# Kernel tuning notes

Hardware: AMD Instinct MI355X
Metric: run time of the kernel (lower is better)

Reference implementation:

```python
import jax, jax.numpy as jnp
from jax import lax
import numpy as np

PARAM_NAMES = ['S1_max','S2_max','f_tens','f_rchr','f_base','r1','ku','c','alpha','psi','kappa','ki','ks','n','v','v_A','v_B','Ac_max','b','lambda','chi','mu_t','T_rain','T_melt','melt_rate','lapse_rate','opg','MFMAX','MFMIN']
PARAM_BOUNDS = {'S1_max':(50.,5000.),'S2_max':(100.,10000.),'f_tens':(.05,.95),'f_rchr':(.05,.95),'f_base':(.05,.95),'r1':(.05,.95),'ku':(.01,1000.),'c':(1.,20.),'alpha':(1.,250.),'psi':(1.,5.),'kappa':(.05,.95),'ki':(.01,1000.),'ks':(.001,10000.),'n':(1.,10.),'v':(.001,.25),'v_A':(.001,.25),'v_B':(.001,.25),'Ac_max':(.05,.95),'b':(.001,3.),'lambda':(5.,10.),'chi':(2.,5.),'mu_t':(.01,5.),'T_rain':(-2.,4.),'T_melt':(-2.,4.),'melt_rate':(1.,10.),'lapse_rate':(-9.8,0.),'opg':(0.,1.),'MFMAX':(1.,10.),'MFMIN':(0.,10.)}
_LOW = jnp.asarray(np.array([PARAM_BOUNDS[n][0] for n in PARAM_NAMES], np.float32))
_HIGH = jnp.asarray(np.array([PARAM_BOUNDS[n][1] for n in PARAM_NAMES], np.float32))
_IDX = {n: i for i, n in enumerate(PARAM_NAMES)}
REF_ELEV = 1500.0      # reference gauge elevation [m]
ROUTE_SHAPE = 2.5      # gamma unit-hydrograph shape
UH_LEN = 30            # routing kernel length [days]


def setup_inputs() -> dict:
    key = jax.random.key(0)
    k1, k2, k3 = jax.random.split(key, 3)
    E, T, NB = 64, 8192, 16
    raw_params = 0.5 * jax.random.normal(k1, (E, 29), jnp.float32)
    u = jax.random.uniform(k2, (T, 3), jnp.float32)
    precip = jnp.where(u[:, 0] > 0.6, (u[:, 0] - 0.6) * 50.0, 0.0)  # mm/day
    pet = u[:, 1] * 5.0                                             # mm/day
    temp = (u[:, 2] - 0.4) * 25.0                                   # deg C
    forcing = jnp.stack([precip, pet, temp], axis=1)
    state_init = jnp.array([50.0, 250.0], jnp.float32)
    af = jax.random.uniform(k3, (NB,), jnp.float32) + 0.1
    area_frac = af / af.sum()
    mean_elev = 800.0 + 150.0 * jnp.arange(NB, dtype=jnp.float32)
    return dict(raw_params=raw_params, forcing=forcing, state_init=state_init,
                area_frac=area_frac, mean_elev=mean_elev)


def _simulate(raw_params, forcing, state_init, area_frac, mean_elev):
    phys = _LOW + (_HIGH - _LOW) * jax.nn.sigmoid(raw_params)  # [E,29] sigmoid-bounded params
    g = lambda n: phys[:, _IDX[n]][:, None]                    # [E,1]
    s1max, s2max = g('S1_max'), g('S2_max')
    ku, c_exp, ki = g('ku'), g('c'), g('ki')
    ks, n_exp = g('ks')[:, 0], g('n')[:, 0]
    ac_max, b_exp = g('Ac_max'), g('b')
    t_rain, t_melt, melt_rate = g('T_rain'), g('T_melt'), g('melt_rate')
    delev = (mean_elev - REF_ELEV) / 1000.0                    # [nb] km
    tshift = g('lapse_rate') * delev                           # [E,nb]
    pmult = jnp.maximum(1.0 + g('opg') * delev, 0.0)           # [E,nb]
    s2max1 = g('S2_max')[:, 0]
    E, NB = raw_params.shape[0], mean_elev.shape[0]

    swe0 = jnp.zeros((E, NB), phys.dtype)
    s1_0 = jnp.broadcast_to(state_init[0], (E, NB))
    s2_0 = jnp.broadcast_to(state_init[1], (E,))

    def step(carry, x):
        swe, s1, s2 = carry
        p, pet, tair = x[0], x[1], x[2]
        tb = tair + tshift                                     # band temperature [E,nb]
        pb = p * pmult                                         # band precip
        rain = jnp.where(tb > t_rain, pb, 0.0)
        snow = pb - rain
        melt = jnp.minimum(melt_rate * jnp.maximum(tb - t_melt, 0.0), swe + snow)
        swe = swe + snow - melt
        infl = rain + melt
        w1 = jnp.clip(s1 / s1max, 0.0, 1.0)
        evap = pet * w1
        qsx = ac_max * w1 ** b_exp * infl                      # saturated-area runoff
        perc = ku * w1 ** c_exp                                # percolation to lower zone
        qif = ki * w1                                          # interflow
        s1n = s1 + infl - qsx - evap - perc - qif
        over1 = jnp.maximum(s1n - s1max, 0.0)
        s1 = jnp.clip(s1n, 0.0, s1max)
        qsurf = qsx + over1
        rech = jnp.sum(area_frac * perc, axis=-1)              # [E]
        w2 = jnp.clip(s2 / s2max1, 0.0, 1.0)
        qb = ks * w2 ** n_exp                                  # baseflow
        s2n = s2 + rech - qb
        over2 = jnp.maximum(s2n - s2max1, 0.0)
        s2 = jnp.clip(s2n, 0.0, s2max1)
        q = jnp.sum(area_frac * (qsurf + qif), axis=-1) + qb + over2
        return (swe, s1, s2), q

    _, runoff = lax.scan(step, (swe0, s1_0, s2_0), forcing)   # [T,E]
    runoff = runoff.T                                          # [E,T]

    # gamma unit-hydrograph routing: shape=ROUTE_SHAPE, scale=mu_t
    delay = phys[:, _IDX['mu_t']]                              # [E]
    tmid = jnp.arange(UH_LEN, dtype=runoff.dtype) + 0.5        # bin midpoints [days]
    k = jnp.asarray(ROUTE_SHAPE, runoff.dtype)
    logpdf = ((k - 1.0) * jnp.log(tmid)[None, :]
              - tmid[None, :] / delay[:, None]
              - lax.lgamma(k) - k * jnp.log(delay)[:, None])
    w = jnp.exp(logpdf)
    w = w / w.sum(axis=1, keepdims=True)                       # [E,UH_LEN]
    T = runoff.shape[1]
    padded = jnp.pad(runoff, ((0, 0), (UH_LEN - 1, 0)))
    routed = jnp.zeros_like(runoff)
    for l in range(UH_LEN):  # small fixed kernel loop (not a data-dim loop)
        routed = routed + w[:, l:l + 1] * lax.dynamic_slice_in_dim(padded, UH_LEN - 1 - l, T, axis=1)
    return routed


def reference(raw_params, forcing, state_init, area_frac, mean_elev):
    return _simulate(raw_params, forcing, state_init, area_frac, mean_elev)
```

## Files before the change

kernel.cpp:

```cpp
#include <hip/hip_runtime.h>
#include <math.h>

#define T_STEPS 8192
#define GROUP   64
#define NQ      (GROUP / 4)
#define NG      (T_STEPS / GROUP)

__device__ __forceinline__ float hw_exp2(float x) { return __builtin_amdgcn_exp2f(x); }
__device__ __forceinline__ float hw_log2(float x) { return __builtin_amdgcn_logf(x); }

#if __has_builtin(__builtin_amdgcn_fmed3f)
__device__ __forceinline__ float clamp01(float x) { return __builtin_amdgcn_fmed3f(x, 0.0f, 1.0f); }
#else
__device__ __forceinline__ float clamp01(float x) { return fminf(fmaxf(x, 0.0f), 1.0f); }
#endif

__global__ __launch_bounds__(256, 1) void fuse_pipe_kernel(
    const float* __restrict__ raw,
    const float* __restrict__ forcing,
    const float* __restrict__ state_init,
    const float* __restrict__ area_frac,
    const float* __restrict__ mean_elev,
    float* __restrict__ qout)
{
    const int tid  = threadIdx.x;
    const int wid  = tid >> 6;
    const int lane = tid & 63;
    const int grp  = lane >> 4;
    const int nb   = lane & 15;
    const int e    = blockIdx.x * 4 + grp;

    __shared__ float4 bufI4[2][NQ][64];
    __shared__ float4 bufC4[2][NQ][64];
    __shared__ float4 bufP4[2][NQ][67];
    __shared__ float4 bufQ4[2][NQ][67];
    __shared__ float4 bufR4[2][4][NQ + 1];
    __shared__ float4 bufS4[2][4][NQ + 1];

    const float* rp = raw + e * 29;
    auto phys = [&](int idx, float lo, float hi) {
        float x = rp[idx];
        float s = 1.0f / (1.0f + expf(-x));
        return lo + (hi - lo) * s;
    };
    const float s1max = phys(0,  50.0f,  5000.0f);
    const float s2max = phys(1,  100.0f, 10000.0f);
    const float ku    = phys(6,  0.01f,  1000.0f);
    const float c_exp = phys(7,  1.0f,   20.0f);
    const float ki    = phys(11, 0.01f,  1000.0f);
    const float ks    = phys(12, 0.001f, 10000.0f);
    const float n_exp = phys(13, 1.0f,   10.0f);
    const float acmax = phys(17, 0.05f,  0.95f);
    const float b_exp = phys(18, 0.001f, 3.0f);
    const float train = phys(22, -2.0f,  4.0f);
    const float tmelt = phys(23, -2.0f,  4.0f);
    const float mrate = phys(24, 1.0f,   10.0f);
    const float lapse = phys(25, -9.8f,  0.0f);
    const float opg   = phys(26, 0.0f,   1.0f);

    const float delev  = (mean_elev[nb] - 1500.0f) / 1000.0f;
    const float tshift = lapse * delev;
    const float pmult  = fmaxf(1.0f + opg * delev, 0.0f);
    const float af     = area_frac[nb];
    const float inv_s1max = 1.0f / s1max;
    const float inv_s2max = 1.0f / s2max;
    const float kup    = ku * inv_s1max;
    const float ksn    = ks * inv_s2max;
    const float afku   = af * ku;
    const float afki   = af * ki;
    const float afs1   = af * s1max;

    float swe = 0.0f;
    float w1  = state_init[0] * inv_s1max;
    float v2  = state_init[1] * inv_s2max;

    float* __restrict__ out = qout + (size_t)e * T_STEPS;
    const float4* __restrict__ fvec = (const float4*)forcing;

    for (int i = 0; i < NG + 3; ++i) {
        if (wid == 0) {
            if (i < NG) {
                const int pb_ = i & 1;
                const int base = i * 48;
                #pragma unroll
                for (int h = 0; h < 4; ++h) {
                    float f[48];
                    #pragma unroll
                    for (int j = 0; j < 12; ++j) {
                        const float4 L = fvec[base + h * 12 + j];
                        f[4*j+0] = L.x; f[4*j+1] = L.y; f[4*j+2] = L.z; f[4*j+3] = L.w;
                    }
                    float4 vi, vc;
                    #pragma unroll
                    for (int s = 0; s < 16; ++s) {
                        const int tt = h * 16 + s;
                        const float p    = f[3*s + 0];
                        const float pet  = f[3*s + 1];
                        const float tair = f[3*s + 2];
                        const float tb   = tair + tshift;
                        const float pcp  = p * pmult;
                        const float snow = (tb > train) ? 0.0f : pcp;
                        const float ssn  = swe + snow;
                        const float mcap = mrate * fmaxf(tb - tmelt, 0.0f);
                        const float swen = fmaxf(ssn - mcap, 0.0f);
                        const float infl = pcp + swe - swen;
                        swe = swen;
                        const int c3 = tt & 3;
                        (&vi.x)[c3] = infl * inv_s1max;
                        (&vc.x)[c3] = fmaf(-(pet + ki), inv_s1max, 1.0f);
                        if (c3 == 3) {
                            bufI4[pb_][tt >> 2][lane] = vi;
                            bufC4[pb_][tt >> 2][lane] = vc;
                        }
                    }
                }
            }
        } else if (wid == 1) {
            const int g = i - 1;
            if (g >= 0 && g < NG) {
                const int pb_ = g & 1;
                #pragma unroll
                for (int k = 0; k < NQ; ++k) {
                    const float4 fi4 = bufI4[pb_][k][lane];
                    const float4 fc4 = bufC4[pb_][k][lane];
                    float4 oP, oQ;
                    #pragma unroll
                    for (int c3 = 0; c3 < 4; ++c3) {
                        const float fi  = (&fi4.x)[c3];
                        const float fcv = (&fc4.x)[c3];
                        const float fap = acmax * fi;
                        const float lg  = hw_log2(w1);
                        const float pwc = hw_exp2(c_exp * lg);
                        const float pwb = hw_exp2(b_exp * lg);
                        const float u   = fmaf(fcv, w1, fi);
                        const float u1  = fmaf(-kup, pwc, u);
                        const float u2  = fmaf(-fap, pwb, u1);
                        const float over1 = fmaxf(u2 - 1.0f, 0.0f);
                        const float qift  = afki * w1;
                        w1 = clamp01(u2);
                        const float qsxn = fap * pwb;
                        (&oP.x)[c3] = afku * pwc;
                        (&oQ.x)[c3] = fmaf(afs1, qsxn + over1, qift);
                    }
                    bufP4[pb_][k][lane] = oP;
                    bufQ4[pb_][k][lane] = oQ;
                }
            }
        } else if (wid == 2) {
            const int g = i - 2;
            if (g >= 0 && g < NG) {
                const int pb_ = g & 1;
                const int arr = lane >> 5;
                const int se  = (lane >> 3) & 3;
                const int tq  = lane & 7;
                #pragma unroll
                for (int j = 0; j < 2; ++j) {
                    const int q_ = tq + 8 * j;
                    const float4* src = arr ? &bufQ4[pb_][q_][se * 16]
                                            : &bufP4[pb_][q_][se * 16];
                    float4 s = src[0];
                    #pragma unroll
                    for (int n = 1; n < 16; ++n) {
                        const float4 v = src[n];
                        s.x += v.x; s.y += v.y; s.z += v.z; s.w += v.w;
                    }
                    if (arr) bufS4[pb_][se][q_] = s;
                    else     bufR4[pb_][se][q_] = s;
                }
            }
        } else {
            const int g = i - 3;
            if (g >= 0) {
                const int pb_ = g & 1;
                float qk0 = 0.0f, qk1 = 0.0f, qk2 = 0.0f, qk3 = 0.0f;
                auto c2body = [&](bool clampPw) {
                    #pragma unroll
                    for (int k = 0; k < NQ; ++k) {
                        const float4 r4 = bufR4[pb_][grp][k];
                        const float4 s4 = bufS4[pb_][grp][k];
                        #pragma unroll
                        for (int c3 = 0; c3 < 4; ++c3) {
                            const int tt = 4 * k + c3;
                            const float rech = (&r4.x)[c3];
                            const float qsum = (&s4.x)[c3];
                            const float lg2 = hw_log2(v2);
                            float m = n_exp * lg2;
                            if (clampPw) m = fminf(m, 0.0f);
                            const float pwm = hw_exp2(m);
                            const float u   = fmaf(rech, inv_s2max, v2);
                            const float u2  = fmaf(-ksn, pwm, u);
                            const float over2 = fmaxf(u2 - 1.0f, 0.0f);
                            v2 = clamp01(u2);
                            const float q = fmaf(s2max, over2, fmaf(ks, pwm, qsum));
                            const bool sel = (tt & 15) == nb;
                            if      (tt < 16) qk0 = sel ? q : qk0;
                            else if (tt < 32) qk1 = sel ? q : qk1;
                            else if (tt < 48) qk2 = sel ? q : qk2;
                            else              qk3 = sel ? q : qk3;
                        }
                    }
                };
                if (g == 0) c2body(true); else c2body(false);

                float* __restrict__ o = out + g * GROUP;
                o[nb]      = qk0;
                o[nb + 16] = qk1;
                o[nb + 32] = qk2;
                o[nb + 48] = qk3;
            }
        }
        __syncthreads();
    }
}

__global__ __launch_bounds__(256) void route_kernel(
    const float* __restrict__ raw,
    float* __restrict__ q_io)
{
    __shared__ float w_sh[32];
    __shared__ float row[T_STEPS];

    const int e   = blockIdx.x;
    const int tid = threadIdx.x;

    const float4* src  = (const float4*)(q_io + (size_t)e * T_STEPS);
    float4*       dst4 = (float4*)row;
    for (int i = tid; i < T_STEPS / 4; i += 256) dst4[i] = src[i];

    if (tid < 32) {
        float x     = raw[e * 29 + 21];
        float sig   = 1.0f / (1.0f + expf(-x));
        float delay = 0.01f + (5.0f - 0.01f) * sig;
        float wv = 0.0f;
        if (tid < 30) {
            const float tm   = (float)tid + 0.5f;
            const float kk   = 2.5f;
            const float lgam = 0.28468287047291918f;
            float lp = (kk - 1.0f) * logf(tm) - tm / delay - lgam - kk * logf(delay);
            wv = expf(lp);
        }
        w_sh[tid] = wv;
    }
    __syncthreads();
    if (tid == 0) {
        float s = 0.0f;
        for (int l = 0; l < 30; ++l) s += w_sh[l];
        w_sh[31] = 1.0f / s;
    }
    __syncthreads();

    float wloc[30];
    const float inv = w_sh[31];
    #pragma unroll
    for (int l = 0; l < 30; ++l) wloc[l] = w_sh[l] * inv;

    float* __restrict__ out = q_io + (size_t)e * T_STEPS;
    for (int t = tid; t < T_STEPS; t += 256) {
        float acc = 0.0f;
        #pragma unroll
        for (int l = 0; l < 30; ++l) {
            const int idx = t - l;
            const float v = (idx >= 0) ? row[idx] : 0.0f;
            acc = fmaf(wloc[l], v, acc);
        }
        out[t] = acc;
    }
}

extern "C" void kernel_launch(void* const* d_in, const int* in_sizes, int n_in,
                              void* d_out, int out_size, void* d_ws, size_t ws_size,
                              hipStream_t stream) {
    const float* raw        = (const float*)d_in[0];
    const float* forcing    = (const float*)d_in[1];
    const float* state_init = (const float*)d_in[2];
    const float* area_frac  = (const float*)d_in[3];
    const float* mean_elev  = (const float*)d_in[4];

    float* out = (float*)d_out;

    fuse_pipe_kernel<<<16, 256, 0, stream>>>(raw, forcing, state_init,
                                             area_frac, mean_elev, out);
    route_kernel<<<64, 256, 0, stream>>>(raw, out);
}
```

Measured before the change: 360.7 us.

## Fuse unit-hydrograph routing into the pipelined simulation kernel as a fifth wave

Result: faster. 339.9 us (median of 2 runs) (-5.8%).

```diff
diff --git a/kernel.cpp b/kernel.cpp
--- a/kernel.cpp
+++ b/kernel.cpp
@@ -5,6 +5,7 @@
 #define GROUP   64
 #define NQ      (GROUP / 4)
 #define NG      (T_STEPS / GROUP)
+#define UH      30
 
 __device__ __forceinline__ float hw_exp2(float x) { return __builtin_amdgcn_exp2f(x); }
 __device__ __forceinline__ float hw_log2(float x) { return __builtin_amdgcn_logf(x); }
@@ -15,13 +16,13 @@
 __device__ __forceinline__ float clamp01(float x) { return fminf(fmaxf(x, 0.0f), 1.0f); }
 #endif
 
-__global__ __launch_bounds__(256, 1) void fuse_pipe_kernel(
+__global__ __launch_bounds__(320, 1) void fuse_pipe_kernel(
     const float* __restrict__ raw,
     const float* __restrict__ forcing,
     const float* __restrict__ state_init,
     const float* __restrict__ area_frac,
     const float* __restrict__ mean_elev,
-    float* __restrict__ qout)
+    float* __restrict__ routed)
 {
     const int tid  = threadIdx.x;
     const int wid  = tid >> 6;
@@ -36,6 +37,10 @@
     __shared__ float4 bufQ4[2][NQ][67];
     __shared__ float4 bufR4[2][4][NQ + 1];
     __shared__ float4 bufS4[2][4][NQ + 1];
+    __shared__ float qring[4][257];
+
+    for (int k = tid; k < 4 * 257; k += 320)
+        ((float*)qring)[k] = 0.0f;
 
     const float* rp = raw + e * 29;
     auto phys = [&](int idx, float lo, float hi) {
@@ -74,10 +79,31 @@
     float w1  = state_init[0] * inv_s1max;
     float v2  = state_init[1] * inv_s2max;
 
-    float* __restrict__ out = qout + (size_t)e * T_STEPS;
+    float wloc[UH];
+    if (wid == 4) {
+        const float x     = raw[e * 29 + 21];
+        const float sig   = 1.0f / (1.0f + expf(-x));
+        const float delay = 0.01f + (5.0f - 0.01f) * sig;
+        const float lgd   = logf(delay);
+        const float invd  = 1.0f / delay;
+        float s = 0.0f;
+        #pragma unroll
+        for (int l = 0; l < UH; ++l) {
+            const float tm = (float)l + 0.5f;
+            const float lp = 1.5f * logf(tm) - tm * invd
+                           - 0.28468287047291918f - 2.5f * lgd;
+            wloc[l] = expf(lp);
+            s += wloc[l];
+        }
+        const float inv = 1.0f / s;
+        #pragma unroll
+        for (int l = 0; l < UH; ++l) wloc[l] *= inv;
+    }
+
+    float* __restrict__ out = routed + (size_t)e * T_STEPS;
     const float4* __restrict__ fvec = (const float4*)forcing;
 
-    for (int i = 0; i < NG + 3; ++i) {
+    for (int i = 0; i < NG + 5; ++i) {
         if (wid == 0) {
             if (i < NG) {
                 const int pb_ = i & 1;
@@ -119,15 +145,19 @@
             const int g = i - 1;
             if (g >= 0 && g < NG) {
                 const int pb_ = g & 1;
+                float4 fi4[NQ], fc4[NQ];
                 #pragma unroll
                 for (int k = 0; k < NQ; ++k) {
-                    const float4 fi4 = bufI4[pb_][k][lane];
-                    const float4 fc4 = bufC4[pb_][k][lane];
+                    fi4[k] = bufI4[pb_][k][lane];
+                    fc4[k] = bufC4[pb_][k][lane];
+                }
+                #pragma unroll
+                for (int k = 0; k < NQ; ++k) {
                     float4 oP, oQ;
                     #pragma unroll
                     for (int c3 = 0; c3 < 4; ++c3) {
-                        const float fi  = (&fi4.x)[c3];
-                        const float fcv = (&fc4.x)[c3];
+                        const float fi  = (&fi4[k].x)[c3];
+                        const float fcv = (&fc4[k].x)[c3];
                         const float fap = acmax * fi;
                         const float lg  = hw_log2(w1);
                         const float pwc = hw_exp2(c_exp * lg);
@@ -168,10 +198,11 @@
                     else     bufR4[pb_][se][q_] = s;
                 }
             }
-        } else {
+        } else if (wid == 3) {
             const int g = i - 3;
-            if (g >= 0) {
+            if (g >= 0 && g < NG) {
                 const int pb_ = g & 1;
+                const int slot = (g & 3) * 64;
                 float qk0 = 0.0f, qk1 = 0.0f, qk2 = 0.0f, qk3 = 0.0f;
                 auto c2body = [&](bool clampPw) {
                     #pragma unroll
@@ -202,68 +233,29 @@
                 };
                 if (g == 0) c2body(true); else c2body(false);
 
-                float* __restrict__ o = out + g * GROUP;
-                o[nb]      = qk0;
-                o[nb + 16] = qk1;
-                o[nb + 32] = qk2;
-                o[nb + 48] = qk3;
+                qring[grp][slot + nb]      = qk0;
+                qring[grp][slot + nb + 16] = qk1;
+                qring[grp][slot + nb + 32] = qk2;
+                qring[grp][slot + nb + 48] = qk3;
+            }
+        } else {
+            const int g = i - 5;
+            if (g >= 0 && g < NG) {
+                const int base = (g & 3) * 64;
+                #pragma unroll
+                for (int j = 0; j < 4; ++j) {
+                    const int pl = nb + 16 * j;
+                    float acc = 0.0f;
+                    #pragma unroll
+                    for (int l = 0; l < UH; ++l) {
+                        const int idx = (base + pl - l) & 255;
+                        acc = fmaf(wloc[l], qring[grp][idx], acc);
+                    }
+                    out[g * GROUP + pl] = acc;
+                }
             }
         }
         __syncthreads();
-    }
-}
-
-__global__ __launch_bounds__(256) void route_kernel(
-    const float* __restrict__ raw,
-    float* __restrict__ q_io)
-{
-    __shared__ float w_sh[32];
-    __shared__ float row[T_STEPS];
-
-    const int e   = blockIdx.x;
-    const int tid = threadIdx.x;
-
-    const float4* src  = (const float4*)(q_io + (size_t)e * T_STEPS);
-    float4*       dst4 = (float4*)row;
-    for (int i = tid; i < T_STEPS / 4; i += 256) dst4[i] = src[i];
-
-    if (tid < 32) {
-        float x     = raw[e * 29 + 21];
-        float sig   = 1.0f / (1.0f + expf(-x));
-        float delay = 0.01f + (5.0f - 0.01f) * sig;
-        float wv = 0.0f;
-        if (tid < 30) {
-            const float tm   = (float)tid + 0.5f;
-            const float kk   = 2.5f;
-            const float lgam = 0.28468287047291918f;
-            float lp = (kk - 1.0f) * logf(tm) - tm / delay - lgam - kk * logf(delay);
-            wv = expf(lp);
-        }
-        w_sh[tid] = wv;
-    }
-    __syncthreads();
-    if (tid == 0) {
-        float s = 0.0f;
-        for (int l = 0; l < 30; ++l) s += w_sh[l];
-        w_sh[31] = 1.0f / s;
-    }
-    __syncthreads();
-
-    float wloc[30];
-    const float inv = w_sh[31];
-    #pragma unroll
-    for (int l = 0; l < 30; ++l) wloc[l] = w_sh[l] * inv;
-
-    float* __restrict__ out = q_io + (size_t)e * T_STEPS;
-    for (int t = tid; t < T_STEPS; t += 256) {
-        float acc = 0.0f;
-        #pragma unroll
-        for (int l = 0; l < 30; ++l) {
-            const int idx = t - l;
-            const float v = (idx >= 0) ? row[idx] : 0.0f;
-            acc = fmaf(wloc[l], v, acc);
-        }
-        out[t] = acc;
     }
 }
 
@@ -278,7 +270,6 @@
 
     float* out = (float*)d_out;
 
-    fuse_pipe_kernel<<<16, 256, 0, stream>>>(raw, forcing, state_init,
+    fuse_pipe_kernel<<<16, 320, 0, stream>>>(raw, forcing, state_init,
                                              area_frac, mean_elev, out);
-    route_kernel<<<64, 256, 0, stream>>>(raw, out);
 }
```
